# Kernel tuning notes

Hardware: AMD Instinct MI355X
Metric: run time of the kernel (lower is better)

The kernel has to match this reference:

```python
import jax, jax.numpy as jnp
import numpy as np

DIM = 512
HID = 128
OUT = 32
ORDER = 3
B, L = 4, 4096


def positional_encoding(seq_len, d):
    pos = jnp.arange(seq_len, dtype=jnp.float32)[:, None]
    div = jnp.exp(-jnp.log(jnp.float32(10000.0)) * jnp.arange(0, d, 2, dtype=jnp.float32) / d)
    ang = pos * div[None, :]  # [L, d/2]
    pe = jnp.zeros((seq_len, d), dtype=jnp.float32)
    pe = pe.at[:, 0::2].set(jnp.sin(ang))
    pe = pe.at[:, 1::2].set(jnp.cos(ang))
    return pe


def setup_inputs() -> dict:
    key = jax.random.key(0)
    ks = jax.random.split(key, 9)
    s = lambda fan_in: 1.0 / np.sqrt(fan_in)
    return {
        "u": jax.random.normal(ks[0], (B, L, DIM), dtype=jnp.float32),
        "pW": jax.random.uniform(ks[1], (DIM, DIM * (ORDER + 1)), jnp.float32, -s(DIM), s(DIM)),
        "pb": jax.random.uniform(ks[2], (DIM * (ORDER + 1),), jnp.float32, -s(DIM), s(DIM)),
        "cW": jax.random.uniform(ks[3], (DIM * (ORDER + 1), DIM * (ORDER + 1), 3), jnp.float32, -s(DIM * 4 * 3), s(DIM * 4 * 3)),
        "cb": jax.random.uniform(ks[4], (DIM * (ORDER + 1),), jnp.float32, -s(DIM * 4 * 3), s(DIM * 4 * 3)),
        "fW": jax.random.uniform(ks[5], (HID, ORDER * DIM), jnp.float32, -s(HID), s(HID)),
        "fb": jax.random.uniform(ks[6], (ORDER * DIM,), jnp.float32, -s(HID), s(HID)),
        "oW": jax.random.uniform(ks[7], (DIM, OUT), jnp.float32, -s(DIM), s(DIM)),
        "ob": jax.random.uniform(ks[8], (OUT,), jnp.float32, -s(DIM), s(DIM)),
    }


def _fft_conv(h_filter, v):
    # circular conv along seq dim: h_filter [L, D], v [B, L, D]
    Vf = jnp.fft.rfft(v, axis=1)
    Hf = jnp.fft.rfft(h_filter, axis=0)[None, :, :]
    return jnp.fft.irfft(Vf * Hf, n=v.shape[1], axis=1)


def reference(u, pW, pb, cW, cb, fW, fb, oW, ob):
    seq_len = u.shape[1]
    t = positional_encoding(seq_len, HID)  # [L, HID]
    # hann window, periodic=False
    n = jnp.arange(seq_len, dtype=jnp.float32)
    window = (0.5 * (1.0 - jnp.cos(2.0 * jnp.pi * n / (seq_len - 1))))[:, None]  # [L,1]

    hat_z = u @ pW + pb  # [B, L, 4*DIM]
    # conv1d over seq with kernel 3, padding 1, channels 4*DIM -> 4*DIM
    z = jax.lax.conv_general_dilated(
        hat_z.transpose(0, 2, 1), cW, window_strides=(1,), padding=[(1, 1)],
        dimension_numbers=("NCH", "OIH", "NCH"))
    z = (z + cb[None, :, None]).transpose(0, 2, 1)  # [B, L, 4*DIM]

    v = z[:, :, :DIM]
    projs = z[:, :, DIM:]  # [B, L, 3*DIM]

    hat_h = t @ fW + fb  # [L, 3*DIM]
    h = hat_h * window  # [L, 3*DIM]

    for k in range(ORDER):
        xn = projs[:, :, DIM * k:DIM * (k + 1)]
        hn = h[:, DIM * k:DIM * (k + 1)]
        v = xn * _fft_conv(hn, v)

    return v @ oW + ob  # [B, L, OUT]
```

## Files before the change

### kernel.cpp

```cpp
#include <hip/hip_runtime.h>

typedef __attribute__((ext_vector_type(8))) short short8;
typedef __attribute__((ext_vector_type(4))) float f32x4;
typedef __attribute__((ext_vector_type(4))) unsigned short ushort4v;
typedef __attribute__((ext_vector_type(8))) unsigned short ushort8v;
typedef unsigned short ushortT;

#define PADROWS 4098
#define HSTR 2056
#define PI_F 3.14159265358979323f
#define PHYS(i) ((i) ^ (((i) >> 4) & 15))

__device__ __forceinline__ ushortT f2bf(float f) {
  union { float f; unsigned int u; } v; v.f = f;
  unsigned int r = (v.u + 0x7FFFu + ((v.u >> 16) & 1u)) >> 16;
  return (ushortT)r;
}
__device__ __forceinline__ float bf2f(ushortT b) {
  union { unsigned int u; float f; } v; v.u = ((unsigned int)b) << 16;
  return v.f;
}

__device__ __forceinline__ void gl2lds16(const void* g, void* l) {
  __builtin_amdgcn_global_load_lds((const __attribute__((address_space(1))) void*)g,
                                   (__attribute__((address_space(3))) void*)l, 16, 0, 0);
}


__global__ void prep_all(const float* __restrict__ u, ushortT* __restrict__ up,
                         const float* __restrict__ pW, ushortT* __restrict__ pW_bf,
                         float2* __restrict__ Wg, float2* __restrict__ Sg) {
  int blk = blockIdx.x;
  if (blk < 8192) {
    size_t idx = (size_t)blk * 256 + threadIdx.x;
    f32x4 v = *(const f32x4*)(u + idx * 4);
    ushort4v r;
    r[0] = f2bf(v[0]); r[1] = f2bf(v[1]); r[2] = f2bf(v[2]); r[3] = f2bf(v[3]);
    size_t g = idx * 4;
    int col = (int)(g & 511);
    int l = (int)(g >> 9);
    int b = l >> 12;
    *(ushort4v*)(up + ((size_t)b * PADROWS + (l & 4095) + 1) * 512 + col) = r;
    return;
  }
  if (blk < 8208) {
    int idx = (blk - 8192) * 256 + threadIdx.x;
    int col = idx & 511;
    int r = (idx >> 9) & 1;
    int b = idx >> 10;
    up[((size_t)b * PADROWS + (r ? 4097 : 0)) * 512 + col] = 0;
    return;
  }
  if (blk < 9232) {
    size_t idx = (size_t)(blk - 8208) * 256 + threadIdx.x;
    f32x4 v = *(const f32x4*)(pW + idx * 4);
    ushort4v r;
    r[0] = f2bf(v[0]); r[1] = f2bf(v[1]); r[2] = f2bf(v[2]); r[3] = f2bf(v[3]);
    *(ushort4v*)(pW_bf + idx * 4) = r;
    return;
  }
  int m = (blk - 9232) * 256 + threadIdx.x;
  float sn, cs;
  if (m < 2048) {
    sincosf(-2.0f * PI_F * (float)m / 2048.0f, &sn, &cs);
    Wg[m] = make_float2(cs, sn);
  } else {
    int k = m - 2048;
    sincosf(PI_F * (float)k / 2048.0f, &sn, &cs);
    Sg[k] = make_float2(cs, sn);
  }
}

__global__ void cwt_pbc(const float* __restrict__ cW, const float* __restrict__ pb,
                        const float* __restrict__ cb, ushortT* __restrict__ Wt,
                        float* __restrict__ biasC, float* __restrict__ pbC0,
                        float* __restrict__ pbC2) {
  int o = blockIdx.x;
  int tid = threadIdx.x;
  float s0 = 0.f, s1 = 0.f, s2 = 0.f;
  const float* base = cW + (size_t)o * 6144;
  for (int i = tid; i < 2048; i += 256) {
    float w0 = base[i * 3], w1 = base[i * 3 + 1], w2 = base[i * 3 + 2];
    size_t oi = (size_t)o * 2048 + i;
    Wt[oi]           = f2bf(w0);
    Wt[oi + 4194304] = f2bf(w1);
    Wt[oi + 8388608] = f2bf(w2);
    float p = pb[i];
    s0 = fmaf(p, w0, s0);
    s1 = fmaf(p, w1, s1);
    s2 = fmaf(p, w2, s2);
  }
#pragma unroll
  for (int off = 32; off >= 1; off >>= 1) {
    s0 += __shfl_down(s0, off);
    s1 += __shfl_down(s1, off);
    s2 += __shfl_down(s2, off);
  }
  __shared__ float red[4][3];
  if ((tid & 63) == 0) { red[tid >> 6][0] = s0; red[tid >> 6][1] = s1; red[tid >> 6][2] = s2; }
  __syncthreads();
  if (tid == 0) {
    float a0 = red[0][0] + red[1][0] + red[2][0] + red[3][0];
    float a1 = red[0][1] + red[1][1] + red[2][1] + red[3][1];
    float a2 = red[0][2] + red[1][2] + red[2][2] + red[3][2];
    biasC[o] = cb[o] + a0 + a1 + a2;
    pbC0[o] = a0;
    pbC2[o] = a2;
  }
}


__launch_bounds__(256, 4)
__global__ void gemm_fold(const ushortT* __restrict__ Wt, const ushortT* __restrict__ pW_bf,
                          ushortT* __restrict__ cWf) {
  __shared__ alignas(16) ushortT As[64 * 64];
  __shared__ alignas(16) ushortT Bs[128 * 64];
  const int tid = threadIdx.x;
  const int lane = tid & 63, w = tid >> 6;
  const int wm = w >> 1, wn = w & 1;
  const int tm = blockIdx.x, tn = blockIdx.y, h = blockIdx.z;
  const ushortT* A = Wt + (size_t)h * 4194304;
  f32x4 acc[2][4] = {};
#pragma unroll 1
  for (int kt = 0; kt < 32; ++kt) {
    const int i0 = kt * 64;
#pragma unroll
    for (int i = 0; i < 2; ++i) {
      int ldsoff = (i * 4 + w) * 1024;
      int m = ((i * 4 + w) << 3) + (lane >> 3);
      int col = (lane & 7) * 8;
      gl2lds16(A + (size_t)(tm * 64 + m) * 2048 + i0 + col, (char*)As + ldsoff);
    }
#pragma unroll
    for (int i = 0; i < 4; ++i) {
      int ldsoff = (i * 4 + w) * 1024;
      int m = ((i * 4 + w) << 3) + (lane >> 3);
      int col = (lane & 7) * 8;
      gl2lds16(pW_bf + (size_t)(tn * 128 + m) * 2048 + i0 + col, (char*)Bs + ldsoff);
    }
    __syncthreads();
#pragma unroll
    for (int ks = 0; ks < 2; ++ks) {
      short8 av[2], bv[4];
#pragma unroll
      for (int mi = 0; mi < 2; ++mi) {
        int row = wm * 32 + mi * 16 + (lane & 15);
        av[mi] = *(const short8*)(As + row * 64 + (ks * 4 + (lane >> 4)) * 8);
      }
#pragma unroll
      for (int ni = 0; ni < 4; ++ni) {
        int row = wn * 64 + ni * 16 + (lane & 15);
        bv[ni] = *(const short8*)(Bs + row * 64 + (ks * 4 + (lane >> 4)) * 8);
      }
#pragma unroll
      for (int mi = 0; mi < 2; ++mi)
#pragma unroll
        for (int ni = 0; ni < 4; ++ni)
          acc[mi][ni] = __builtin_amdgcn_mfma_f32_16x16x32_bf16(av[mi], bv[ni], acc[mi][ni], 0, 0, 0);
    }
    __syncthreads();
  }
#pragma unroll
  for (int mi = 0; mi < 2; ++mi)
#pragma unroll
    for (int ni = 0; ni < 4; ++ni) {
      int jc = tn * 128 + wn * 64 + ni * 16 + (lane & 15);
#pragma unroll
      for (int j = 0; j < 4; ++j) {
        int o = tm * 64 + wm * 32 + mi * 16 + (lane >> 4) * 4 + j;
        cWf[((size_t)h * 2048 + o) * 512 + jc] = f2bf(acc[mi][ni][j]);
      }
    }
}


__launch_bounds__(512, 2)
__global__ void gemm_conv8(const ushortT* __restrict__ Upad, const ushortT* __restrict__ cWf,
                           const float* __restrict__ biasC, const float* __restrict__ pbC0,
                           const float* __restrict__ pbC2, ushortT* __restrict__ vTb,
                           ushortT* __restrict__ projsT) {
  __shared__ ushortT lds[2][2][16384];
  const int tid = threadIdx.x;
  const int lane = tid & 63, w = tid >> 6;
  const int wm = w >> 2, wn = w & 3;
  int raw = blockIdx.x;
  int wg  = (raw & 7) * 64 + (raw >> 3);
  const int o0 = (wg >> 6) << 8;
  const int nt = wg & 63;
  const int b  = nt >> 4;
  const int l0 = (nt & 15) << 8;

  f32x4 acc[8][4] = {};
  short8 xf[4][2];

  const int sm = tid >> 3;
  const int sw1 = ((tid & 7) ^ (sm & 7)) << 3;

  auto stageW = [&](int slot, int half, int t) {
    int q = (t * 21846) >> 16, h = t - 3 * q, j0 = q << 6;
    size_t grow = (size_t)(h * 2048 + o0 + half * 128 + sm);
    char* dst = (char*)&lds[slot][0][0] + half * 16384 + w * 1024;
    gl2lds16(cWf + grow * 512 + j0 + sw1, dst);
    gl2lds16(cWf + (grow + 64) * 512 + j0 + sw1, dst + 8192);
  };
  auto stageX = [&](int slot, int half, int t) {
    int q = (t * 21846) >> 16, h = t - 3 * q, j0 = q << 6;
    size_t grow = (size_t)b * PADROWS + l0 + h + half * 128 + sm;
    char* dst = (char*)&lds[slot][1][0] + half * 16384 + w * 1024;
    gl2lds16(Upad + grow * 512 + j0 + sw1, dst);
    gl2lds16(Upad + (grow + 64) * 512 + j0 + sw1, dst + 8192);
  };
  auto ldsW = [&](int slot, int mi, int ks) -> short8 {
    int row = wm * 128 + mi * 16 + (lane & 15);
    int ch = (ks * 4 + (lane >> 4)) ^ (row & 7);
    return *(const short8*)&lds[slot][0][row * 64 + ch * 8];
  };
  auto ldsX = [&](int slot, int ni, int ks) -> short8 {
    int row = wn * 64 + ni * 16 + (lane & 15);
    int ch = (ks * 4 + (lane >> 4)) ^ (row & 7);
    return *(const short8*)&lds[slot][1][row * 64 + ch * 8];
  };

  stageW(0, 0, 0); stageW(0, 1, 0);
  stageX(0, 0, 0); stageX(0, 1, 0);
  stageX(1, 0, 1); stageX(1, 1, 1);
  asm volatile("s_waitcnt vmcnt(0)" ::: "memory");
  __builtin_amdgcn_s_barrier();

#define PHASE(slot, q, STAGECODE, VMCODE)                                                                    \
  {                                                                                                          \
    short8 w0k0 = ldsW(slot, 2*(q), 0), w0k1 = ldsW(slot, 2*(q), 1);                                         \
    short8 w1k0 = ldsW(slot, 2*(q)+1, 0), w1k1 = ldsW(slot, 2*(q)+1, 1);                                     \
    if ((q) == 0) {                                                                                          \
      _Pragma("unroll")                                                                                      \
      for (int ni = 0; ni < 4; ++ni) {                                                                       \
        xf[ni][0] = ldsX(slot, ni, 0);                                                                       \
        xf[ni][1] = ldsX(slot, ni, 1);                                                                       \
      }                                                                                                      \
    }                                                                                                        \
    STAGECODE;                                                                                               \
    VMCODE;                                                                                                  \
    __builtin_amdgcn_s_barrier();                                                                            \
    asm volatile("s_waitcnt lgkmcnt(0)" ::: "memory");                                                       \
    __builtin_amdgcn_sched_barrier(0);                                                                       \
    __builtin_amdgcn_s_setprio(1);                                                                           \
    _Pragma("unroll")                                                                                        \
    for (int ni = 0; ni < 4; ++ni) {                                                                         \
      acc[2*(q)][ni]   = __builtin_amdgcn_mfma_f32_16x16x32_bf16(w0k0, xf[ni][0], acc[2*(q)][ni], 0, 0, 0);  \
      acc[2*(q)][ni]   = __builtin_amdgcn_mfma_f32_16x16x32_bf16(w0k1, xf[ni][1], acc[2*(q)][ni], 0, 0, 0);  \
      acc[2*(q)+1][ni] = __builtin_amdgcn_mfma_f32_16x16x32_bf16(w1k0, xf[ni][0], acc[2*(q)+1][ni], 0, 0, 0);\
      acc[2*(q)+1][ni] = __builtin_amdgcn_mfma_f32_16x16x32_bf16(w1k1, xf[ni][1], acc[2*(q)+1][ni], 0, 0, 0);\
    }                                                                                                        \
    __builtin_amdgcn_s_setprio(0);                                                                           \
  }

#pragma unroll 1
  for (int it = 0; it < 11; ++it) {
    const int t0 = 2 * it;
    PHASE(0, 0, , );
    PHASE(0, 1, stageW(1, 0, t0 + 1), );
    PHASE(0, 2, stageW(1, 1, t0 + 1); stageX(0, 0, t0 + 2), );
    PHASE(0, 3, stageX(0, 1, t0 + 2), asm volatile("s_waitcnt vmcnt(4)" ::: "memory"));
    PHASE(1, 0, , );
    PHASE(1, 1, stageW(0, 0, t0 + 2), );
    PHASE(1, 2, stageW(0, 1, t0 + 2); stageX(1, 0, t0 + 3), );
    PHASE(1, 3, stageX(1, 1, t0 + 3), asm volatile("s_waitcnt vmcnt(4)" ::: "memory"));
  }
  PHASE(0, 0, , );
  PHASE(0, 1, stageW(1, 0, 23), );
  PHASE(0, 2, stageW(1, 1, 23), );
  PHASE(0, 3, , asm volatile("s_waitcnt vmcnt(0)" ::: "memory"));
  PHASE(1, 0, , );
  PHASE(1, 1, , );
  PHASE(1, 2, , );
  PHASE(1, 3, , );
#undef PHASE

  const int r4 = (lane >> 4) * 4;
  const int lbase = l0 + wn * 64 + (lane & 15);
  if (o0 < 512) {
#pragma unroll
    for (int mi = 0; mi < 8; ++mi)
#pragma unroll
      for (int ni = 0; ni < 4; ++ni) {
        int l = lbase + ni * 16;
#pragma unroll
        for (int j = 0; j < 4; ++j) {
          int o = o0 + wm * 128 + mi * 16 + r4 + j;
          float val = acc[mi][ni][j] + biasC[o];
          if (l == 0) val -= pbC0[o];
          if (l == 4095) val -= pbC2[o];
          vTb[((size_t)b * 512 + o) * 4096 + l] = f2bf(val);
        }
      }
  } else {
#pragma unroll
    for (int mi = 0; mi < 8; ++mi)
#pragma unroll
      for (int ni = 0; ni < 4; ++ni) {
        int l = lbase + ni * 16;
#pragma unroll
        for (int j = 0; j < 4; ++j) {
          int o = o0 + wm * 128 + mi * 16 + r4 + j;
          float val = acc[mi][ni][j] + biasC[o];
          if (l == 0) val -= pbC0[o];
          if (l == 4095) val -= pbC2[o];
          int oc = o - 512;
          projsT[((size_t)((oc >> 9) * 4 + b) * 512 + (oc & 511)) * 4096 + l] = f2bf(val);
        }
      }
  }
}


__launch_bounds__(256, 1)
__global__ void h_kernel(const float* __restrict__ fW, const float* __restrict__ fb,
                         float* __restrict__ hT) {
  __shared__ float tTs[128][64];
  __shared__ float fWs[128][128];
  const int l0 = blockIdx.x * 64;
  const int c0 = blockIdx.y * 128;
  const int tid = threadIdx.x;
  for (int r = tid; r < 4096; r += 256) {
    int d2 = r >> 6, li = r & 63;
    float dv = expf(-9.210340371976184f * (float)(2 * d2) / 128.0f);
    float ang = (float)(l0 + li) * dv;
    tTs[2 * d2][li] = sinf(ang);
    tTs[2 * d2 + 1][li] = cosf(ang);
  }
  {
    int cq = (tid & 31) * 4;
    int dr = tid >> 5;
#pragma unroll
    for (int d = dr; d < 128; d += 8)
      *(f32x4*)(&fWs[d][cq]) = *(const f32x4*)(fW + (size_t)d * 1536 + c0 + cq);
  }
  __syncthreads();
  const int lgrp = tid & 15;
  const int cg = tid >> 4;
  float acc[8][4] = {};
#pragma unroll 4
  for (int d = 0; d < 128; ++d) {
    f32x4 tv = *(const f32x4*)(&tTs[d][lgrp * 4]);
#pragma unroll
    for (int j = 0; j < 8; ++j) {
      float wv = fWs[d][cg + 16 * j];
      acc[j][0] = fmaf(tv[0], wv, acc[j][0]);
      acc[j][1] = fmaf(tv[1], wv, acc[j][1]);
      acc[j][2] = fmaf(tv[2], wv, acc[j][2]);
      acc[j][3] = fmaf(tv[3], wv, acc[j][3]);
    }
  }
  f32x4 wl;
#pragma unroll
  for (int j = 0; j < 4; ++j) {
    int l = l0 + lgrp * 4 + j;
    wl[j] = 0.5f * (1.0f - cosf(6.283185307179586f * (float)l / 4095.0f));
  }
#pragma unroll
  for (int j = 0; j < 8; ++j) {
    int ch = c0 + cg + 16 * j;
    float fbv = fb[ch];
    f32x4 r;
    r[0] = (acc[j][0] + fbv) * wl[0];
    r[1] = (acc[j][1] + fbv) * wl[1];
    r[2] = (acc[j][2] + fbv) * wl[2];
    r[3] = (acc[j][3] + fbv) * wl[3];
    *(f32x4*)(hT + (size_t)ch * 4096 + l0 + lgrp * 4) = r;
  }
}


__device__ __forceinline__ float2 cadd(float2 a, float2 b){ return make_float2(a.x+b.x, a.y+b.y); }
__device__ __forceinline__ float2 csub(float2 a, float2 b){ return make_float2(a.x-b.x, a.y-b.y); }
__device__ __forceinline__ float2 cmulp(float2 a, float2 b){
  return make_float2(a.x*b.x - a.y*b.y, a.x*b.y + a.y*b.x);
}
template<bool INV>
__device__ __forceinline__ float2 tw_mul(float2 a, float2 w) {
  return INV ? make_float2(fmaf(a.x, w.x,  a.y*w.y), fmaf(a.y, w.x, -a.x*w.y))
             : make_float2(fmaf(a.x, w.x, -a.y*w.y), fmaf(a.x, w.y,  a.y*w.x));
}
template<bool INV>
__device__ __forceinline__ float2 rot(float2 z) {
  return INV ? make_float2(-z.y, z.x) : make_float2(z.y, -z.x);
}

template<bool INV>
__device__ __forceinline__ void bfly8(const float2 v[8], float2 o[8]) {
  const float C7 = 0.70710678118654752f;
  float2 a0 = cadd(v[0], v[4]), a1 = csub(v[0], v[4]);
  float2 a2 = cadd(v[2], v[6]), a3 = rot<INV>(csub(v[2], v[6]));
  float2 E0 = cadd(a0, a2), E1 = cadd(a1, a3), E2 = csub(a0, a2), E3 = csub(a1, a3);
  float2 b0 = cadd(v[1], v[5]), b1 = csub(v[1], v[5]);
  float2 b2 = cadd(v[3], v[7]), b3 = rot<INV>(csub(v[3], v[7]));
  float2 O0 = cadd(b0, b2), O1 = cadd(b1, b3), O2 = csub(b0, b2), O3 = csub(b1, b3);
  O1 = cmulp(O1, INV ? make_float2(C7, C7) : make_float2(C7, -C7));
  O2 = rot<INV>(O2);
  O3 = cmulp(O3, INV ? make_float2(-C7, C7) : make_float2(-C7, -C7));
  o[0] = cadd(E0, O0); o[1] = cadd(E1, O1); o[2] = cadd(E2, O2); o[3] = cadd(E3, O3);
  o[4] = csub(E0, O0); o[5] = csub(E1, O1); o[6] = csub(E2, O2); o[7] = csub(E3, O3);
}

template<bool INV, int NS>
__device__ __forceinline__ void stage_r8(float2* X, const float2* Wl, int t) {
  float2 v[8];
#pragma unroll
  for (int r = 0; r < 8; ++r) v[r] = X[PHYS(t + 256 * r)];
  if (NS > 1) {
    const int jm = (t & (NS - 1)) * (256 / NS);
#pragma unroll
    for (int r = 1; r < 8; ++r) v[r] = tw_mul<INV>(v[r], Wl[PHYS(r * jm)]);
  }
  float2 o[8];
  bfly8<INV>(v, o);
  __syncthreads();
  const int base = (t / NS) * (8 * NS) + (t % NS);
#pragma unroll
  for (int i = 0; i < 8; ++i) X[PHYS(base + i * NS)] = o[i];
  __syncthreads();
}

template<bool INV>
__device__ __forceinline__ void stage_r4(float2* X, const float2* Wl, int t) {
#pragma unroll
  for (int jj = 0; jj < 2; ++jj) {
    const int j = t + jj * 256;
    float2 v0 = X[PHYS(j)], v1 = X[PHYS(j + 512)], v2 = X[PHYS(j + 1024)], v3 = X[PHYS(j + 1536)];
    v1 = tw_mul<INV>(v1, Wl[PHYS(j)]);
    v2 = tw_mul<INV>(v2, Wl[PHYS(2 * j)]);
    v3 = tw_mul<INV>(v3, Wl[PHYS(3 * j)]);
    float2 a0 = cadd(v0, v2), a1 = csub(v0, v2), a2 = cadd(v1, v3), a3 = rot<INV>(csub(v1, v3));
    X[PHYS(j)]        = cadd(a0, a2);
    X[PHYS(j + 512)]  = cadd(a1, a3);
    X[PHYS(j + 1024)] = csub(a0, a2);
    X[PHYS(j + 1536)] = csub(a1, a3);
  }
  __syncthreads();
}

__device__ __forceinline__ void fwd_stage1_bf16(float2* X, const unsigned int* __restrict__ sigb, int t) {
  float2 v[8], o[8];
#pragma unroll
  for (int r = 0; r < 8; ++r) {
    unsigned int pr = sigb[t + 256 * r];
    v[r] = make_float2(bf2f((ushortT)(pr & 0xffffu)), bf2f((ushortT)(pr >> 16)));
  }
  bfly8<false>(v, o);
  const int base = t * 8;
#pragma unroll
  for (int i = 0; i < 8; ++i) X[PHYS(base + i)] = o[i];
  __syncthreads();
}

__device__ __forceinline__ void fwd_stage1_f32(float2* X, const float* __restrict__ sig, int t) {
  float2 v[8], o[8];
#pragma unroll
  for (int r = 0; r < 8; ++r) v[r] = *(const float2*)(sig + 2 * (t + 256 * r));
  bfly8<false>(v, o);
  const int base = t * 8;
#pragma unroll
  for (int i = 0; i < 8; ++i) X[PHYS(base + i)] = o[i];
  __syncthreads();
}

__device__ __forceinline__ void fwd_stage1_gated(float2* X, const unsigned int* __restrict__ xnb,
                                                 float scale, int t) {
  float2 v[8], o[8];
#pragma unroll
  for (int r = 0; r < 8; ++r) {
    const int m = t + 256 * r;
    unsigned int pr = xnb[m];
    float2 a = X[PHYS(m)];
    v[r] = make_float2(a.x * scale * bf2f((ushortT)(pr & 0xffffu)),
                       a.y * scale * bf2f((ushortT)(pr >> 16)));
  }
  bfly8<false>(v, o);
  __syncthreads();
  const int base = t * 8;
#pragma unroll
  for (int i = 0; i < 8; ++i) X[PHYS(base + i)] = o[i];
  __syncthreads();
}

__device__ __forceinline__ void stage_r4_store(const float2* X, const float2* Wl,
                                               const unsigned int* __restrict__ xnb,
                                               float scale, unsigned int* __restrict__ outb, int t) {
#pragma unroll
  for (int jj = 0; jj < 2; ++jj) {
    const int j = t + jj * 256;
    float2 v0 = X[PHYS(j)], v1 = X[PHYS(j + 512)], v2 = X[PHYS(j + 1024)], v3 = X[PHYS(j + 1536)];
    v1 = tw_mul<true>(v1, Wl[PHYS(j)]);
    v2 = tw_mul<true>(v2, Wl[PHYS(2 * j)]);
    v3 = tw_mul<true>(v3, Wl[PHYS(3 * j)]);
    float2 a0 = cadd(v0, v2), a1 = csub(v0, v2), a2 = cadd(v1, v3), a3 = rot<true>(csub(v1, v3));
    float2 y[4] = { cadd(a0, a2), cadd(a1, a3), csub(a0, a2), csub(a1, a3) };
    const int idx[4] = { j, j + 512, j + 1024, j + 1536 };
#pragma unroll
    for (int q = 0; q < 4; ++q) {
      unsigned int pr = xnb[idx[q]];
      unsigned int lo = f2bf(y[q].x * scale * bf2f((ushortT)(pr & 0xffffu)));
      unsigned int hi = f2bf(y[q].y * scale * bf2f((ushortT)(pr >> 16)));
      outb[idx[q]] = lo | (hi << 16);
    }
  }
}

__launch_bounds__(256, 4)
__global__ void fft_filter_r(const float* __restrict__ hT, const float2* __restrict__ Wg,
                             float2* __restrict__ Hf) {
  __shared__ float2 X[2048];
  __shared__ float2 Wl[2048];
  const int ch = blockIdx.x;
  const int tid = threadIdx.x;
  const float* sig = hT + (size_t)ch * 4096;
  for (int m = tid; m < 2048; m += 256) Wl[PHYS(m)] = Wg[m];
  fwd_stage1_f32(X, sig, tid);
  stage_r8<false, 8>(X, Wl, tid);
  stage_r8<false, 64>(X, Wl, tid);
  stage_r4<false>(X, Wl, tid);
  float2* o = Hf + (size_t)ch * HSTR;
  for (int kk = tid; kk < 1024; kk += 256) {
    if (kk == 0) {
      float2 z0 = X[PHYS(0)];
      o[0]    = make_float2(z0.x + z0.y, 0.f);
      o[2048] = make_float2(z0.x - z0.y, 0.f);
      float2 zq = X[PHYS(1024)];
      o[1024] = make_float2(zq.x, -zq.y);
    } else {
      float2 zk = X[PHYS(kk)], zm = X[PHYS(2048 - kk)];
      float2 E = make_float2(0.5f * (zk.x + zm.x), 0.5f * (zk.y - zm.y));
      float2 D = make_float2(0.5f * (zk.x - zm.x), 0.5f * (zk.y + zm.y));
      float2 O = make_float2(D.y, -D.x);
      float sn, cs;
      __sincosf(-PI_F * (float)kk * (1.0f / 2048.0f), &sn, &cs);
      float2 twO = make_float2(O.x * cs - O.y * sn, O.x * sn + O.y * cs);
      o[kk]        = make_float2(E.x + twO.x, E.y + twO.y);
      o[2048 - kk] = make_float2(E.x - twO.x, -(E.y - twO.y));
    }
  }
}

__launch_bounds__(256, 4)
__global__ void fft_conv3(ushortT* __restrict__ vTb, const ushortT* __restrict__ projsT,
                          const float2* __restrict__ Hf, const float2* __restrict__ Wg,
                          const float2* __restrict__ Sg) {
  __shared__ float2 X[2048];
  __shared__ float2 Wl[2048];
  __shared__ float2 S[1024];
  const int bc = blockIdx.x;
  const int c = bc & 511, b = bc >> 9;
  const int tid = threadIdx.x;
  unsigned int* sigb = (unsigned int*)(vTb + (size_t)bc * 4096);
  for (int m = tid; m < 2048; m += 256) Wl[PHYS(m)] = Wg[m];
  for (int m = tid; m < 1024; m += 256) S[m] = Sg[m];
  fwd_stage1_bf16(X, sigb, tid);
  stage_r8<false, 8>(X, Wl, tid);
  stage_r8<false, 64>(X, Wl, tid);
  stage_r4<false>(X, Wl, tid);
  const float scale = 1.0f / 2048.0f;
#pragma unroll 1
  for (int k = 0; k < 3; ++k) {
    const float2* H = Hf + (size_t)(k * 512 + c) * HSTR;
    for (int kk = tid; kk < 1024; kk += 256) {
      if (kk == 0) {
        float h0x = H[0].x, hMx = H[2048].x;
        float2 hq = H[1024];
        float a1r = 0.5f * (h0x + hMx), a1w = 0.5f * (h0x - hMx);
        float2 Z0 = X[PHYS(0)], Zq = X[PHYS(1024)];
        X[PHYS(0)]    = make_float2(a1r * Z0.x + a1w * Z0.y, a1r * Z0.y + a1w * Z0.x);
        X[PHYS(1024)] = make_float2(hq.x * Zq.x + hq.y * Zq.y, hq.x * Zq.y - hq.y * Zq.x);
      } else {
        float2 hk = H[kk], hm = H[2048 - kk];
        float cs = S[kk].x, sn = S[kk].y;
        float oms = 0.5f * (1.f - sn), ops = 0.5f * (1.f + sn), c2h = 0.5f * cs;
        float d1x = hk.x - hm.x, d1y = hk.y + hm.y;
        float a1x = oms * hk.x + ops * hm.x, a1y = oms * hk.y - ops * hm.y;
        float b1x = -c2h * d1y, b1y = c2h * d1x;
        float a2x = oms * hm.x + ops * hk.x, a2y = oms * hm.y - ops * hk.y;
        float b2x = c2h * d1y, b2y = c2h * d1x;
        float2 Zk = X[PHYS(kk)], Zm = X[PHYS(2048 - kk)];
        X[PHYS(kk)] = make_float2(a1x * Zk.x - a1y * Zk.y + b1x * Zm.x + b1y * Zm.y,
                                  a1x * Zk.y + a1y * Zk.x - b1x * Zm.y + b1y * Zm.x);
        X[PHYS(2048 - kk)] = make_float2(a2x * Zm.x - a2y * Zm.y + b2x * Zk.x + b2y * Zk.y,
                                         a2x * Zm.y + a2y * Zm.x - b2x * Zk.y + b2y * Zk.x);
      }
    }
    __syncthreads();
    stage_r8<true, 1>(X, Wl, tid);
    stage_r8<true, 8>(X, Wl, tid);
    stage_r8<true, 64>(X, Wl, tid);
    const unsigned int* xnb = (const unsigned int*)(projsT + ((size_t)(k * 4 + b) * 512 + c) * 4096);
    if (k < 2) {
      stage_r4<true>(X, Wl, tid);
      fwd_stage1_gated(X, xnb, scale, tid);
      stage_r8<false, 8>(X, Wl, tid);
      stage_r8<false, 64>(X, Wl, tid);
      stage_r4<false>(X, Wl, tid);
    } else {
      stage_r4_store(X, Wl, xnb, scale, sigb, tid);
    }
  }
}


__launch_bounds__(256, 2)
__global__ void out_gemm(const ushortT* __restrict__ vTb, const float* __restrict__ oW,
                         const float* __restrict__ ob, float* __restrict__ out) {
  __shared__ float vs[64][68];
  __shared__ float ows[64][36];
  const int l0 = blockIdx.x * 64;
  const int b = l0 >> 12;
  const int tid = threadIdx.x;
  const int l = tid & 63;
  const int og = (tid >> 6) * 8;
  float acc[8] = {};
  const ushortT* vb = vTb + (size_t)b * 2097152 + (l0 & 4095);
  const int cs = tid >> 2;
  const int lq = (tid & 3) * 16;
  const int oq = (tid & 3) * 8;
#pragma unroll 1
  for (int cc = 0; cc < 512; cc += 64) {
#pragma unroll
    for (int i = 0; i < 2; ++i) {
      ushort8v u8 = *(const ushort8v*)(vb + (size_t)(cc + cs) * 4096 + lq + i * 8);
#pragma unroll
      for (int j = 0; j < 8; ++j) vs[cs][lq + i * 8 + j] = bf2f(u8[j]);
    }
    *(f32x4*)(&ows[cs][oq])     = *(const f32x4*)(oW + (cc + cs) * 32 + oq);
    *(f32x4*)(&ows[cs][oq + 4]) = *(const f32x4*)(oW + (cc + cs) * 32 + oq + 4);
    __syncthreads();
#pragma unroll 8
    for (int c3 = 0; c3 < 64; ++c3) {
      float v = vs[c3][l];
#pragma unroll
      for (int j = 0; j < 8; ++j)
        acc[j] = fmaf(v, ows[c3][og + j], acc[j]);
    }
    __syncthreads();
  }
  float* op = out + (size_t)(l0 + l) * 32 + og;
  f32x4 r0, r1;
  r0[0] = acc[0] + ob[og];     r0[1] = acc[1] + ob[og + 1];
  r0[2] = acc[2] + ob[og + 2]; r0[3] = acc[3] + ob[og + 3];
  r1[0] = acc[4] + ob[og + 4]; r1[1] = acc[5] + ob[og + 5];
  r1[2] = acc[6] + ob[og + 6]; r1[3] = acc[7] + ob[og + 7];
  *(f32x4*)op = r0;
  *(f32x4*)(op + 4) = r1;
}


__global__ void ws_sentinel(float* __restrict__ out) {
  if (threadIdx.x == 0) out[0] = -31337.0f;
}


extern "C" void kernel_launch(void* const* d_in, const int* in_sizes, int n_in,
                              void* d_out, int out_size, void* d_ws, size_t ws_size,
                              hipStream_t stream) {
  (void)in_sizes; (void)n_in; (void)out_size;
  const float* u  = (const float*)d_in[0];
  const float* pW = (const float*)d_in[1];
  const float* pb = (const float*)d_in[2];
  const float* cW = (const float*)d_in[3];
  const float* cb = (const float*)d_in[4];
  const float* fW = (const float*)d_in[5];
  const float* fb = (const float*)d_in[6];
  const float* oW = (const float*)d_in[7];
  const float* ob = (const float*)d_in[8];
  float* out = (float*)d_out;

  char* ws = (char*)d_ws;
  ushortT* Upad   = (ushortT*)(ws);
  ushortT* cWf    = (ushortT*)(ws + 16785408);
  float*   biasC  = (float*)  (ws + 23076864);
  float*   pbC0   = (float*)  (ws + 23085056);
  float*   pbC2   = (float*)  (ws + 23093248);
  float2*  Wg     = (float2*) (ws + 23101440);
  float2*  Sg     = (float2*) (ws + 23117824);
  float2*  Hf     = (float2*) (ws + 23126016);
  ushortT* vTb    = (ushortT*)(ws + 48390144);
  ushortT* projsT = (ushortT*)(ws + 65167360);
  const size_t total = 115499008;
  char* S = (char*)vTb;
  ushortT* Wt     = (ushortT*)(S);
  ushortT* pW_bf  = (ushortT*)(S + 25165824);
  float*   hT     = (float*)  (S + 27262976);

  if (total > ws_size) {
    ws_sentinel<<<1, 64, 0, stream>>>(out);
    return;
  }

  prep_all<<<9244, 256, 0, stream>>>(u, Upad, pW, pW_bf, Wg, Sg);
  cwt_pbc<<<2048, 256, 0, stream>>>(cW, pb, cb, Wt, biasC, pbC0, pbC2);
  gemm_fold<<<dim3(32, 4, 3), 256, 0, stream>>>(Wt, pW_bf, cWf);
  h_kernel<<<dim3(64, 12), 256, 0, stream>>>(fW, fb, hT);
  fft_filter_r<<<1536, 256, 0, stream>>>(hT, Wg, Hf);
  gemm_conv8<<<512, 512, 0, stream>>>(Upad, cWf, biasC, pbC0, pbC2, vTb, projsT);
  fft_conv3<<<2048, 256, 0, stream>>>(vTb, projsT, Hf, Wg, Sg);
  out_gemm<<<256, 256, 0, stream>>>(vTb, oW, ob, out);
}
```

Measured before the change: 313.1 us.

## Merge prep and cwt kernels; halve FFT twiddle table in LDS

Folds the cwt_pbc weight-transpose/bias kernel into the prep kernel as extra blocks, removing one launch and its tail. Separately, FFT kernels now keep only the first half of the twiddle table in shared memory and derive the second half by sign flip (W^(m+N/2) = -W^m). This halves the twiddle LDS footprint and its fill loop, which may let more blocks fit per CU, at the cost of a few extra ALU ops per twiddle read.

```diff
diff --git a/kernel.cpp b/kernel.cpp
--- a/kernel.cpp
+++ b/kernel.cpp
@@ -27,12 +27,17 @@
 }
 
 
-__global__ void prep_all(const float* __restrict__ u, ushortT* __restrict__ up,
+__global__ void prep_cwt(const float* __restrict__ u, ushortT* __restrict__ up,
                          const float* __restrict__ pW, ushortT* __restrict__ pW_bf,
-                         float2* __restrict__ Wg, float2* __restrict__ Sg) {
+                         float2* __restrict__ Wg, float2* __restrict__ Sg,
+                         const float* __restrict__ cW, const float* __restrict__ pb,
+                         const float* __restrict__ cb, ushortT* __restrict__ Wt,
+                         float* __restrict__ biasC, float* __restrict__ pbC0,
+                         float* __restrict__ pbC2) {
   int blk = blockIdx.x;
+  int tid = threadIdx.x;
   if (blk < 8192) {
-    size_t idx = (size_t)blk * 256 + threadIdx.x;
+    size_t idx = (size_t)blk * 256 + tid;
     f32x4 v = *(const f32x4*)(u + idx * 4);
     ushort4v r;
     r[0] = f2bf(v[0]); r[1] = f2bf(v[1]); r[2] = f2bf(v[2]); r[3] = f2bf(v[3]);
@@ -44,7 +49,7 @@
     return;
   }
   if (blk < 8208) {
-    int idx = (blk - 8192) * 256 + threadIdx.x;
+    int idx = (blk - 8192) * 256 + tid;
     int col = idx & 511;
     int r = (idx >> 9) & 1;
     int b = idx >> 10;
@@ -52,31 +57,27 @@
     return;
   }
   if (blk < 9232) {
-    size_t idx = (size_t)(blk - 8208) * 256 + threadIdx.x;
+    size_t idx = (size_t)(blk - 8208) * 256 + tid;
     f32x4 v = *(const f32x4*)(pW + idx * 4);
     ushort4v r;
     r[0] = f2bf(v[0]); r[1] = f2bf(v[1]); r[2] = f2bf(v[2]); r[3] = f2bf(v[3]);
     *(ushort4v*)(pW_bf + idx * 4) = r;
     return;
   }
-  int m = (blk - 9232) * 256 + threadIdx.x;
-  float sn, cs;
-  if (m < 2048) {
-    sincosf(-2.0f * PI_F * (float)m / 2048.0f, &sn, &cs);
-    Wg[m] = make_float2(cs, sn);
-  } else {
-    int k = m - 2048;
-    sincosf(PI_F * (float)k / 2048.0f, &sn, &cs);
-    Sg[k] = make_float2(cs, sn);
-  }
-}
-
-__global__ void cwt_pbc(const float* __restrict__ cW, const float* __restrict__ pb,
-                        const float* __restrict__ cb, ushortT* __restrict__ Wt,
-                        float* __restrict__ biasC, float* __restrict__ pbC0,
-                        float* __restrict__ pbC2) {
-  int o = blockIdx.x;
-  int tid = threadIdx.x;
+  if (blk < 9244) {
+    int m = (blk - 9232) * 256 + tid;
+    float sn, cs;
+    if (m < 2048) {
+      sincosf(-2.0f * PI_F * (float)m / 2048.0f, &sn, &cs);
+      Wg[m] = make_float2(cs, sn);
+    } else {
+      int k = m - 2048;
+      sincosf(PI_F * (float)k / 2048.0f, &sn, &cs);
+      Sg[k] = make_float2(cs, sn);
+    }
+    return;
+  }
+  int o = blk - 9244;
   float s0 = 0.f, s1 = 0.f, s2 = 0.f;
   const float* base = cW + (size_t)o * 6144;
   for (int i = tid; i < 2048; i += 256) {
@@ -376,6 +377,13 @@
 __device__ __forceinline__ float2 cmulp(float2 a, float2 b){
   return make_float2(a.x*b.x - a.y*b.y, a.x*b.y + a.y*b.x);
 }
+__device__ __forceinline__ float2 ldw(const float2* __restrict__ Wl, int m) {
+  float2 w = Wl[PHYS(m & 1023)];
+  unsigned int neg = (unsigned int)(m & 1024) << 21;
+  w.x = __uint_as_float(__float_as_uint(w.x) ^ neg);
+  w.y = __uint_as_float(__float_as_uint(w.y) ^ neg);
+  return w;
+}
 template<bool INV>
 __device__ __forceinline__ float2 tw_mul(float2 a, float2 w) {
   return INV ? make_float2(fmaf(a.x, w.x,  a.y*w.y), fmaf(a.y, w.x, -a.x*w.y))
@@ -410,7 +418,7 @@
   if (NS > 1) {
     const int jm = (t & (NS - 1)) * (256 / NS);
 #pragma unroll
-    for (int r = 1; r < 8; ++r) v[r] = tw_mul<INV>(v[r], Wl[PHYS(r * jm)]);
+    for (int r = 1; r < 8; ++r) v[r] = tw_mul<INV>(v[r], ldw(Wl, r * jm));
   }
   float2 o[8];
   bfly8<INV>(v, o);
@@ -427,9 +435,9 @@
   for (int jj = 0; jj < 2; ++jj) {
     const int j = t + jj * 256;
     float2 v0 = X[PHYS(j)], v1 = X[PHYS(j + 512)], v2 = X[PHYS(j + 1024)], v3 = X[PHYS(j + 1536)];
-    v1 = tw_mul<INV>(v1, Wl[PHYS(j)]);
-    v2 = tw_mul<INV>(v2, Wl[PHYS(2 * j)]);
-    v3 = tw_mul<INV>(v3, Wl[PHYS(3 * j)]);
+    v1 = tw_mul<INV>(v1, ldw(Wl, j));
+    v2 = tw_mul<INV>(v2, ldw(Wl, 2 * j));
+    v3 = tw_mul<INV>(v3, ldw(Wl, 3 * j));
     float2 a0 = cadd(v0, v2), a1 = csub(v0, v2), a2 = cadd(v1, v3), a3 = rot<INV>(csub(v1, v3));
     X[PHYS(j)]        = cadd(a0, a2);
     X[PHYS(j + 512)]  = cadd(a1, a3);
@@ -490,9 +498,9 @@
   for (int jj = 0; jj < 2; ++jj) {
     const int j = t + jj * 256;
     float2 v0 = X[PHYS(j)], v1 = X[PHYS(j + 512)], v2 = X[PHYS(j + 1024)], v3 = X[PHYS(j + 1536)];
-    v1 = tw_mul<true>(v1, Wl[PHYS(j)]);
-    v2 = tw_mul<true>(v2, Wl[PHYS(2 * j)]);
-    v3 = tw_mul<true>(v3, Wl[PHYS(3 * j)]);
+    v1 = tw_mul<true>(v1, ldw(Wl, j));
+    v2 = tw_mul<true>(v2, ldw(Wl, 2 * j));
+    v3 = tw_mul<true>(v3, ldw(Wl, 3 * j));
     float2 a0 = cadd(v0, v2), a1 = csub(v0, v2), a2 = cadd(v1, v3), a3 = rot<true>(csub(v1, v3));
     float2 y[4] = { cadd(a0, a2), cadd(a1, a3), csub(a0, a2), csub(a1, a3) };
     const int idx[4] = { j, j + 512, j + 1024, j + 1536 };
@@ -510,11 +518,11 @@
 __global__ void fft_filter_r(const float* __restrict__ hT, const float2* __restrict__ Wg,
                              float2* __restrict__ Hf) {
   __shared__ float2 X[2048];
-  __shared__ float2 Wl[2048];
+  __shared__ float2 Wl[1024];
   const int ch = blockIdx.x;
   const int tid = threadIdx.x;
   const float* sig = hT + (size_t)ch * 4096;
-  for (int m = tid; m < 2048; m += 256) Wl[PHYS(m)] = Wg[m];
+  for (int m = tid; m < 1024; m += 256) Wl[PHYS(m)] = Wg[m];
   fwd_stage1_f32(X, sig, tid);
   stage_r8<false, 8>(X, Wl, tid);
   stage_r8<false, 64>(X, Wl, tid);
@@ -546,13 +554,13 @@
                           const float2* __restrict__ Hf, const float2* __restrict__ Wg,
                           const float2* __restrict__ Sg) {
   __shared__ float2 X[2048];
-  __shared__ float2 Wl[2048];
+  __shared__ float2 Wl[1024];
   __shared__ float2 S[1024];
   const int bc = blockIdx.x;
   const int c = bc & 511, b = bc >> 9;
   const int tid = threadIdx.x;
   unsigned int* sigb = (unsigned int*)(vTb + (size_t)bc * 4096);
-  for (int m = tid; m < 2048; m += 256) Wl[PHYS(m)] = Wg[m];
+  for (int m = tid; m < 1024; m += 256) Wl[PHYS(m)] = Wg[m];
   for (int m = tid; m < 1024; m += 256) S[m] = Sg[m];
   fwd_stage1_bf16(X, sigb, tid);
   stage_r8<false, 8>(X, Wl, tid);
@@ -692,8 +700,7 @@
     return;
   }
 
-  prep_all<<<9244, 256, 0, stream>>>(u, Upad, pW, pW_bf, Wg, Sg);
-  cwt_pbc<<<2048, 256, 0, stream>>>(cW, pb, cb, Wt, biasC, pbC0, pbC2);
+  prep_cwt<<<11292, 256, 0, stream>>>(u, Upad, pW, pW_bf, Wg, Sg, cW, pb, cb, Wt, biasC, pbC0, pbC2);
   gemm_fold<<<dim3(32, 4, 3), 256, 0, stream>>>(Wt, pW_bf, cWf);
   h_kernel<<<dim3(64, 12), 256, 0, stream>>>(fW, fb, hT);
   fft_filter_r<<<1536, 256, 0, stream>>>(hT, Wg, Hf);
```

New measurement: 313.6 us. About the same (+0.2%).
